# Kernel optimization log

Hardware: AMD Instinct MI355X
Metric: run time of the kernel (lower is better)

The kernel has to match this reference:

```python
import jax, jax.numpy as jnp
import numpy as np

L, B, S, C, H, V = 12, 2, 1024, 768, 12, 50257
D = C // H
FF = 4 * C
SCALE = 1.0 / float(np.sqrt(D))


def setup_inputs() -> dict:
    key = jax.random.key(0)
    ks = jax.random.split(key, 10)
    s = 0.02  # GPT-2 init std
    return {
        "idx": jax.random.randint(ks[0], (B, S), 0, V),
        "targets": jax.random.randint(ks[1], (B, S), 0, V),
        "wte": jax.random.normal(ks[2], (V, C), jnp.float32) * s,
        "wpe": jax.random.normal(ks[3], (S, C), jnp.float32) * s,
        "ln1_w": jnp.ones((L, C), jnp.float32),
        "ln1_b": jnp.zeros((L, C), jnp.float32),
        "qkv_w": jax.random.normal(ks[4], (L, C, 3 * C), jnp.float32) * s,
        "qkv_b": jnp.zeros((L, 3 * C), jnp.float32),
        "proj_w": jax.random.normal(ks[5], (L, C, C), jnp.float32) * s,
        "proj_b": jnp.zeros((L, C), jnp.float32),
        "ln2_w": jnp.ones((L, C), jnp.float32),
        "ln2_b": jnp.zeros((L, C), jnp.float32),
        "fc_w": jax.random.normal(ks[6], (L, C, FF), jnp.float32) * s,
        "fc_b": jnp.zeros((L, FF), jnp.float32),
        "fc2_w": jax.random.normal(ks[7], (L, FF, C), jnp.float32) * s,
        "fc2_b": jnp.zeros((L, C), jnp.float32),
        "lnf_w": jnp.ones((C,), jnp.float32),
        "lnf_b": jnp.zeros((C,), jnp.float32),
    }


def _ln(x, w, b):
    m = jnp.mean(x, axis=-1, keepdims=True)
    v = jnp.mean(jnp.square(x - m), axis=-1, keepdims=True)
    return (x - m) * jax.lax.rsqrt(v + 1e-5) * w + b


def _gpt(wte, wpe, ln1_w, ln1_b, qkv_w, qkv_b, proj_w, proj_b,
         ln2_w, ln2_b, fc_w, fc_b, fc2_w, fc2_b, lnf_w, lnf_b, idx, targets):
    h = wte[idx] + wpe[jnp.arange(S)]  # [B,S,C]
    causal = jnp.tril(jnp.ones((S, S), bool))

    def block(h, p):
        l1w, l1b, qw, qb, pw, pb, l2w, l2b, fw, fb, gw, gb = p
        x = _ln(h, l1w, l1b)
        q, k, v = jnp.split(x @ qw + qb, 3, axis=-1)  # each [B,S,C]
        heads = lambda t: t.reshape(B, S, H, D).transpose(0, 2, 1, 3)  # [B,H,S,D]
        q, k, v = heads(q), heads(k), heads(v)
        scores = jnp.einsum('bhsd,bhtd->bhst', q, k) * SCALE
        scores = jnp.where(causal, scores, -jnp.inf)
        att = jax.nn.softmax(scores, axis=-1)
        o = jnp.einsum('bhst,bhtd->bhsd', att, v)
        o = o.transpose(0, 2, 1, 3).reshape(B, S, C)
        h = h + o @ pw + pb
        x = _ln(h, l2w, l2b)
        h = h + jax.nn.gelu(x @ fw + fb, approximate=True) @ gw + gb
        return h, None

    h, _ = jax.lax.scan(block, h, (ln1_w, ln1_b, qkv_w, qkv_b, proj_w, proj_b,
                                   ln2_w, ln2_b, fc_w, fc_b, fc2_w, fc2_b))
    logits = _ln(h, lnf_w, lnf_b) @ wte.T  # tied lm_head, [B,S,V]
    logp = jax.nn.log_softmax(logits, axis=-1)
    loss = -jnp.mean(jnp.take_along_axis(logp, targets[..., None], axis=-1))
    return logits, loss


def reference(idx, targets, wte, wpe, ln1_w, ln1_b, qkv_w, qkv_b, proj_w, proj_b,
              ln2_w, ln2_b, fc_w, fc_b, fc2_w, fc2_b, lnf_w, lnf_b):
    return _gpt(wte, wpe, ln1_w, ln1_b, qkv_w, qkv_b, proj_w, proj_b,
                ln2_w, ln2_b, fc_w, fc_b, fc2_w, fc2_b, lnf_w, lnf_b, idx, targets)
```

## Files before the change

### kernel.cpp

```cpp
#include <hip/hip_runtime.h>
#include <hip/hip_bf16.h>
#include <cstdint>
#include <cstddef>

constexpr int LNUM = 12;
constexpr int BB   = 2;
constexpr int SS   = 1024;
constexpr int CC   = 768;
constexpr int HH   = 12;
constexpr int DD   = 64;
constexpr int FFD  = 3072;
constexpr int VV   = 50257;
constexpr int VPAD = 50304;
constexpr int MM   = BB * SS;
constexpr int NBX  = VPAD / 128;

typedef unsigned short u16;
typedef short     s16x8 __attribute__((ext_vector_type(8)));
typedef float     f32x4 __attribute__((ext_vector_type(4)));
typedef u16       u16x4 __attribute__((ext_vector_type(4)));
typedef u16       u16x8 __attribute__((ext_vector_type(8)));

__device__ __forceinline__ float bf2f(u16 v) {
    return __uint_as_float(((unsigned)v) << 16);
}
__device__ __forceinline__ u16 f2bf(float f) {
    unsigned u = __float_as_uint(f);
    return (u16)((u + 0x7fffu + ((u >> 16) & 1u)) >> 16);
}


__global__ __launch_bounds__(256) void wte_conv_kernel(const float* __restrict__ wte,
                                                       u16* __restrict__ out) {
    size_t i4 = ((size_t)blockIdx.x * 256 + threadIdx.x) * 4;
    if (i4 >= (size_t)VPAD * CC) return;
    size_t r = i4 / CC;
    u16x4 o;
    if (r < (size_t)VV) {
        const float4 v = *(const float4*)&wte[i4];
        o[0] = f2bf(v.x); o[1] = f2bf(v.y); o[2] = f2bf(v.z); o[3] = f2bf(v.w);
    } else {
        o[0] = o[1] = o[2] = o[3] = 0;
    }
    *(u16x4*)&out[i4] = o;
}

__global__ __launch_bounds__(256) void transpose_conv_kernel(const float* __restrict__ in,
                                                             u16* __restrict__ out,
                                                             int R, int Cn) {
    __shared__ float tile[32][33];
    const float* inp = in + (size_t)blockIdx.z * R * Cn;
    u16* outp = out + (size_t)blockIdx.z * R * Cn;
    int c  = blockIdx.x * 32 + threadIdx.x;
    int r0 = blockIdx.y * 32;
#pragma unroll
    for (int i = 0; i < 4; ++i) {
        int r = r0 + threadIdx.y + i * 8;
        tile[threadIdx.y + i * 8][threadIdx.x] = inp[(size_t)r * Cn + c];
    }
    __syncthreads();
    int oc = r0 + threadIdx.x;
#pragma unroll
    for (int i = 0; i < 4; ++i) {
        int orow = blockIdx.x * 32 + threadIdx.y + i * 8;
        outp[(size_t)orow * R + oc] = f2bf(tile[threadIdx.x][threadIdx.y + i * 8]);
    }
}

__global__ __launch_bounds__(256) void embed_kernel(const int* __restrict__ idx,
                                                    const float* __restrict__ wte,
                                                    const float* __restrict__ wpe,
                                                    float* __restrict__ h) {
    int row = blockIdx.x;
    int s   = row & (SS - 1);
    int tok = idx[row];
    const float* we = wte + (size_t)tok * CC;
    const float* pe = wpe + (size_t)s * CC;
    float* hr = h + (size_t)row * CC;
    for (int c = threadIdx.x; c < CC; c += 256) hr[c] = we[c] + pe[c];
}

__global__ __launch_bounds__(256) void ln_kernel(const float* __restrict__ h,
                                                 const float* __restrict__ w,
                                                 const float* __restrict__ b,
                                                 u16* __restrict__ x) {
    int row = blockIdx.x, tid = threadIdx.x;
    const float* hr = h + (size_t)row * CC;
    float v0 = hr[tid], v1 = hr[tid + 256], v2 = hr[tid + 512];
    float s  = v0 + v1 + v2;
    float s2 = v0 * v0 + v1 * v1 + v2 * v2;
#pragma unroll
    for (int off = 32; off; off >>= 1) {
        s  += __shfl_xor(s, off);
        s2 += __shfl_xor(s2, off);
    }
    __shared__ float rs[4], rs2[4], stat[2];
    int wid = tid >> 6;
    if ((tid & 63) == 0) { rs[wid] = s; rs2[wid] = s2; }
    __syncthreads();
    if (tid == 0) {
        float ts  = rs[0] + rs[1] + rs[2] + rs[3];
        float ts2 = rs2[0] + rs2[1] + rs2[2] + rs2[3];
        float mean = ts * (1.0f / CC);
        float var  = ts2 * (1.0f / CC) - mean * mean;
        stat[0] = mean;
        stat[1] = rsqrtf(var + 1e-5f);
    }
    __syncthreads();
    float mean = stat[0], rstd = stat[1];
    size_t base = (size_t)row * CC;
    x[base + tid]       = f2bf((v0 - mean) * rstd * w[tid]       + b[tid]);
    x[base + tid + 256] = f2bf((v1 - mean) * rstd * w[tid + 256] + b[tid + 256]);
    x[base + tid + 512] = f2bf((v2 - mean) * rstd * w[tid + 512] + b[tid + 512]);
}

template <int BM, int BN, int EPI>
__global__ __launch_bounds__(256)
void gemm_bt_kernel(const u16* __restrict__ A, const u16* __restrict__ Bt,
                    const float* __restrict__ bias, float* __restrict__ outf,
                    u16* __restrict__ outb, int K, long long ldo,
                    float* __restrict__ partM, float* __restrict__ partS) {
    constexpr int MR  = BM / 32, NR = BN / 32;
    constexpr int ACH = BM * 64 / (256 * 8);
    constexpr int BCH = BN * 64 / (256 * 8);
    __shared__ u16 As[BM * 64];
    __shared__ u16 Bs[BN * 64];
    const int tid  = threadIdx.x;
    const int lane = tid & 63;
    const int wid  = tid >> 6;
    const int l15  = lane & 15;
    const int lq   = lane >> 4;
    const int wm   = wid & 1;
    const int wn   = wid >> 1;
    const int rx   = l15 & 7;

    const int gx = gridDim.x, gy = gridDim.y;
    const int nwg = gx * gy;
    const int pos = blockIdx.y * gx + blockIdx.x;
    const int qc  = nwg >> 3, rc = nwg & 7;
    const int xcd = pos & 7, cidx = pos >> 3;
    const int wgid = (xcd < rc ? xcd * (qc + 1) : rc * (qc + 1) + (xcd - rc) * qc) + cidx;
    const int bx = wgid / gy, by = wgid % gy;
    const int bm0 = by * BM, bn0 = bx * BN;

    f32x4 acc[MR][NR];
#pragma unroll
    for (int m = 0; m < MR; ++m)
#pragma unroll
        for (int n = 0; n < NR; ++n) acc[m][n] = (f32x4){0.f, 0.f, 0.f, 0.f};

    u16x8 areg[ACH], breg[BCH];
    auto ldreg = [&](int kt) {
#pragma unroll
        for (int it = 0; it < ACH; ++it) {
            int g = it * 256 + tid, r = g >> 3, c = ((g & 7) ^ (r & 7)) * 8;
            areg[it] = *(const u16x8*)&A[(size_t)(bm0 + r) * (size_t)K + kt + c];
        }
#pragma unroll
        for (int it = 0; it < BCH; ++it) {
            int g = it * 256 + tid, r = g >> 3, c = ((g & 7) ^ (r & 7)) * 8;
            breg[it] = *(const u16x8*)&Bt[(size_t)(bn0 + r) * (size_t)K + kt + c];
        }
    };
    auto wlds = [&]() {
#pragma unroll
        for (int it = 0; it < ACH; ++it) *(u16x8*)&As[(it * 256 + tid) * 8] = areg[it];
#pragma unroll
        for (int it = 0; it < BCH; ++it) *(u16x8*)&Bs[(it * 256 + tid) * 8] = breg[it];
    };
    auto compute = [&]() {
#pragma unroll
        for (int ks = 0; ks < 2; ++ks) {
            s16x8 af[MR], bfr[NR];
#pragma unroll
            for (int m = 0; m < MR; ++m) {
                int row = wm * (BM / 2) + m * 16 + l15;
                af[m] = *(const s16x8*)&As[row * 64 + (((ks * 4 + lq) ^ rx) * 8)];
            }
#pragma unroll
            for (int n = 0; n < NR; ++n) {
                int row = wn * (BN / 2) + n * 16 + l15;
                bfr[n] = *(const s16x8*)&Bs[row * 64 + (((ks * 4 + lq) ^ rx) * 8)];
            }
#pragma unroll
            for (int m = 0; m < MR; ++m)
#pragma unroll
                for (int n = 0; n < NR; ++n)
                    acc[m][n] = __builtin_amdgcn_mfma_f32_16x16x32_bf16(af[m], bfr[n], acc[m][n], 0, 0, 0);
        }
    };

    const int nk = K >> 6;
    ldreg(0);
    for (int t = 0; t < nk; ++t) {
        __syncthreads();
        wlds();
        __syncthreads();
        if (t + 1 < nk) ldreg((t + 1) << 6);
        compute();
    }

#pragma unroll
    for (int m = 0; m < MR; ++m) {
#pragma unroll
        for (int n = 0; n < NR; ++n) {
#pragma unroll
            for (int r = 0; r < 4; ++r) {
                int row = bm0 + wm * (BM / 2) + m * 16 + lq * 4 + r;
                int col = bn0 + wn * (BN / 2) + n * 16 + l15;
                float v = acc[m][n][r];
                if (EPI != 3) v += bias[col];
                if (EPI == 1) {
                    float xg = v;
                    v = 0.5f * xg * (1.0f + tanhf(0.7978845608028654f * (xg + 0.044715f * xg * xg * xg)));
                }
                if (EPI == 0 || EPI == 1) {
                    outb[(size_t)row * ldo + col] = f2bf(v);
                } else if (EPI == 2) {
                    outf[(size_t)row * ldo + col] += v;
                } else {
                    if (col < VV) outf[(size_t)row * ldo + col] = v;
                }
            }
        }
    }

    if constexpr (EPI == 3) {
        __shared__ float redM[2][BM], redS[2][BM];
#pragma unroll
        for (int m = 0; m < MR; ++m) {
#pragma unroll
            for (int r = 0; r < 4; ++r) {
                float mx = -3.0e38f;
#pragma unroll
                for (int n = 0; n < NR; ++n) {
                    int colg = bn0 + wn * (BN / 2) + n * 16 + l15;
                    float v = (colg < VV) ? acc[m][n][r] : -3.0e38f;
                    mx = fmaxf(mx, v);
                }
#pragma unroll
                for (int off = 1; off < 16; off <<= 1) mx = fmaxf(mx, __shfl_xor(mx, off));
                float sm = 0.f;
#pragma unroll
                for (int n = 0; n < NR; ++n) {
                    int colg = bn0 + wn * (BN / 2) + n * 16 + l15;
                    if (colg < VV) sm += __expf(acc[m][n][r] - mx);
                }
#pragma unroll
                for (int off = 1; off < 16; off <<= 1) sm += __shfl_xor(sm, off);
                if (l15 == 0) {
                    int rl = wm * (BM / 2) + m * 16 + lq * 4 + r;
                    redM[wn][rl] = mx;
                    redS[wn][rl] = sm;
                }
            }
        }
        __syncthreads();
        if (tid < BM) {
            float m0 = redM[0][tid], m1 = redM[1][tid];
            float M = fmaxf(m0, m1);
            float S = redS[0][tid] * __expf(m0 - M) + redS[1][tid] * __expf(m1 - M);
            size_t rowg = (size_t)(bm0 + tid);
            partM[rowg * NBX + bx] = M;
            partS[rowg * NBX + bx] = S;
        }
    }
}

__global__ __launch_bounds__(256) void attn_mfma_kernel(const u16* __restrict__ qkv,
                                                        u16* __restrict__ o) {
    constexpr int KB = 64, PADC = 72;
    __shared__ u16 Ks[KB][PADC];
    __shared__ u16 Vs[DD][PADC];
    __shared__ u16 Ps[4][16][PADC];

    const int tid = threadIdx.x, lane = tid & 63, wid = tid >> 6;
    const int l15 = lane & 15, lq = lane >> 4;
    const int blk = blockIdx.x;
    const int q0  = (blk & (SS / 64 - 1)) * 64;
    const int bh  = blk / (SS / 64);
    const int b   = bh / HH, hh = bh % HH;

    const size_t base = (size_t)b * SS * (3 * CC);
    const u16* qp = qkv + base + hh * DD;
    const u16* kp = qkv + base + CC + hh * DD;
    const u16* vp = qkv + base + 2 * CC + hh * DD;

    s16x8 qf[2];
    {
        const u16* qr = qp + (size_t)(q0 + wid * 16 + l15) * (3 * CC);
        qf[0] = *(const s16x8*)&qr[lq * 8];
        qf[1] = *(const s16x8*)&qr[32 + lq * 8];
    }

    float m[4], lsum[4];
    f32x4 acc_o[4];
#pragma unroll
    for (int r = 0; r < 4; ++r) { m[r] = -3.0e38f; lsum[r] = 0.f; }
#pragma unroll
    for (int nd = 0; nd < 4; ++nd) acc_o[nd] = (f32x4){0.f, 0.f, 0.f, 0.f};

    const int tend = q0 + 64;
    for (int t0 = 0; t0 < tend; t0 += KB) {
        __syncthreads();
#pragma unroll
        for (int it = 0; it < 2; ++it) {
            int g = it * 256 + tid;
            int t = g >> 3, dc = g & 7;
            *(u16x8*)&Ks[t][dc * 8] = *(const u16x8*)&kp[(size_t)(t0 + t) * (3 * CC) + dc * 8];
        }
#pragma unroll
        for (int it = 0; it < 2; ++it) {
            int g = it * 256 + tid;
            int t = g >> 3, dc = g & 7;
            u16x8 v = *(const u16x8*)&vp[(size_t)(t0 + t) * (3 * CC) + dc * 8];
#pragma unroll
            for (int e = 0; e < 8; ++e) Vs[dc * 8 + e][t] = v[e];
        }
        __syncthreads();

        f32x4 acc_s[4];
#pragma unroll
        for (int n = 0; n < 4; ++n) acc_s[n] = (f32x4){0.f, 0.f, 0.f, 0.f};
#pragma unroll
        for (int ks = 0; ks < 2; ++ks) {
#pragma unroll
            for (int n = 0; n < 4; ++n) {
                s16x8 kb = *(const s16x8*)&Ks[n * 16 + l15][ks * 32 + lq * 8];
                acc_s[n] = __builtin_amdgcn_mfma_f32_16x16x32_bf16(qf[ks], kb, acc_s[n], 0, 0, 0);
            }
        }

#pragma unroll
        for (int n = 0; n < 4; ++n) {
            int colg = t0 + n * 16 + l15;
#pragma unroll
            for (int r = 0; r < 4; ++r) {
                int rowg = q0 + wid * 16 + lq * 4 + r;
                float sv = acc_s[n][r] * 0.125f;
                acc_s[n][r] = (colg <= rowg) ? sv : -3.0e38f;
            }
        }
        float mt[4];
#pragma unroll
        for (int r = 0; r < 4; ++r)
            mt[r] = fmaxf(fmaxf(acc_s[0][r], acc_s[1][r]), fmaxf(acc_s[2][r], acc_s[3][r]));
#pragma unroll
        for (int off = 1; off < 16; off <<= 1)
#pragma unroll
            for (int r = 0; r < 4; ++r) mt[r] = fmaxf(mt[r], __shfl_xor(mt[r], off));

        float rs[4];
#pragma unroll
        for (int r = 0; r < 4; ++r) {
            float mn  = fmaxf(m[r], mt[r]);
            float scl = __expf(m[r] - mn);
            m[r] = mn;
            float ps = 0.f;
#pragma unroll
            for (int n = 0; n < 4; ++n) {
                float p = __expf(acc_s[n][r] - mn);
                acc_s[n][r] = p;
                ps += p;
            }
            rs[r] = ps;
            lsum[r] *= scl;
#pragma unroll
            for (int nd = 0; nd < 4; ++nd) acc_o[nd][r] *= scl;
        }
#pragma unroll
        for (int off = 1; off < 16; off <<= 1)
#pragma unroll
            for (int r = 0; r < 4; ++r) rs[r] += __shfl_xor(rs[r], off);
#pragma unroll
        for (int r = 0; r < 4; ++r) lsum[r] += rs[r];

#pragma unroll
        for (int n = 0; n < 4; ++n)
#pragma unroll
            for (int r = 0; r < 4; ++r)
                Ps[wid][lq * 4 + r][n * 16 + l15] = f2bf(acc_s[n][r]);
        __syncthreads();

#pragma unroll
        for (int ks = 0; ks < 2; ++ks) {
            s16x8 pa = *(const s16x8*)&Ps[wid][l15][ks * 32 + lq * 8];
#pragma unroll
            for (int nd = 0; nd < 4; ++nd) {
                s16x8 vb = *(const s16x8*)&Vs[nd * 16 + l15][ks * 32 + lq * 8];
                acc_o[nd] = __builtin_amdgcn_mfma_f32_16x16x32_bf16(pa, vb, acc_o[nd], 0, 0, 0);
            }
        }
    }

#pragma unroll
    for (int r = 0; r < 4; ++r) {
        float inv = 1.f / lsum[r];
        int rowg = q0 + wid * 16 + lq * 4 + r;
        u16* orow = o + ((size_t)b * SS + rowg) * CC + hh * DD;
#pragma unroll
        for (int nd = 0; nd < 4; ++nd)
            orow[nd * 16 + l15] = f2bf(acc_o[nd][r] * inv);
    }
}

__global__ __launch_bounds__(256) void lse_kernel(const float* __restrict__ partM,
                                                  const float* __restrict__ partS,
                                                  const float* __restrict__ logits,
                                                  const int* __restrict__ tgt,
                                                  float* __restrict__ lossp) {
    int row = blockIdx.x, tid = threadIdx.x;
    float m = -3.0e38f, s = 0.f;
    for (int i = tid; i < NBX; i += 256) {
        float pm = partM[(size_t)row * NBX + i];
        float ps = partS[(size_t)row * NBX + i];
        float nm = fmaxf(m, pm);
        s = s * __expf(m - nm) + ps * __expf(pm - nm);
        m = nm;
    }
#pragma unroll
    for (int off = 32; off; off >>= 1) {
        float om = __shfl_xor(m, off), os = __shfl_xor(s, off);
        float nm = fmaxf(m, om);
        s = s * __expf(m - nm) + os * __expf(om - nm);
        m = nm;
    }
    __shared__ float rm[4], rsh[4];
    int wid = tid >> 6;
    if ((tid & 63) == 0) { rm[wid] = m; rsh[wid] = s; }
    __syncthreads();
    if (tid == 0) {
        float M = fmaxf(fmaxf(rm[0], rm[1]), fmaxf(rm[2], rm[3]));
        float S = rsh[0] * __expf(rm[0] - M) + rsh[1] * __expf(rm[1] - M) +
                  rsh[2] * __expf(rm[2] - M) + rsh[3] * __expf(rm[3] - M);
        float lse = M + __logf(S);
        lossp[row] = lse - logits[(size_t)row * VV + tgt[row]];
    }
}

__global__ __launch_bounds__(256) void loss_reduce_kernel(const float* __restrict__ lossp,
                                                          float* __restrict__ out) {
    int tid = threadIdx.x;
    float s = 0.f;
    for (int i = tid; i < MM; i += 256) s += lossp[i];
#pragma unroll
    for (int off = 32; off; off >>= 1) s += __shfl_xor(s, off);
    __shared__ float r[4];
    if ((tid & 63) == 0) r[tid >> 6] = s;
    __syncthreads();
    if (tid == 0) out[0] = (r[0] + r[1] + r[2] + r[3]) * (1.0f / MM);
}

extern "C" void kernel_launch(void* const* d_in, const int* in_sizes, int n_in,
                              void* d_out, int out_size, void* d_ws, size_t ws_size,
                              hipStream_t stream) {
    const int*   idx     = (const int*)  d_in[0];
    const int*   targets = (const int*)  d_in[1];
    const float* wte     = (const float*)d_in[2];
    const float* wpe     = (const float*)d_in[3];
    const float* ln1w    = (const float*)d_in[4];
    const float* ln1b    = (const float*)d_in[5];
    const float* qkvw    = (const float*)d_in[6];
    const float* qkvbi   = (const float*)d_in[7];
    const float* projw   = (const float*)d_in[8];
    const float* projbi  = (const float*)d_in[9];
    const float* ln2w    = (const float*)d_in[10];
    const float* ln2b    = (const float*)d_in[11];
    const float* fcw     = (const float*)d_in[12];
    const float* fcbi    = (const float*)d_in[13];
    const float* fc2w    = (const float*)d_in[14];
    const float* fc2bi   = (const float*)d_in[15];
    const float* lnfw    = (const float*)d_in[16];
    const float* lnfb    = (const float*)d_in[17];
    float* logits = (float*)d_out;

    char* wsb = (char*)d_ws;
    size_t off = 0;
    auto alloc = [&](size_t n) -> char* {
        char* p = wsb + off;
        off = (off + n + 255) & ~(size_t)255;
        return p;
    };
    u16*   wteT  = (u16*)  alloc((size_t)VPAD * CC * 2);
    u16*   qkvT  = (u16*)  alloc((size_t)LNUM * 3 * CC * CC * 2);
    u16*   projT = (u16*)  alloc((size_t)LNUM * CC * CC * 2);
    u16*   fcT   = (u16*)  alloc((size_t)LNUM * FFD * CC * 2);
    u16*   fc2T  = (u16*)  alloc((size_t)LNUM * CC * FFD * 2);
    float* h     = (float*)alloc((size_t)MM * CC * 4);
    u16*   xb    = (u16*)  alloc((size_t)MM * CC * 2);
    u16*   qkvb  = (u16*)  alloc((size_t)MM * 3 * CC * 2);
    u16*   ob    = (u16*)  alloc((size_t)MM * CC * 2);
    u16*   gb    = (u16*)  alloc((size_t)MM * FFD * 2);
    float* lossp = (float*)alloc((size_t)MM * 4);
    float* partM = (float*)alloc((size_t)MM * NBX * 4);
    float* partS = (float*)alloc((size_t)MM * NBX * 4);

    {
        int blocks = (int)(((size_t)VPAD * CC / 4 + 255) / 256);
        wte_conv_kernel<<<blocks, 256, 0, stream>>>(wte, wteT);
    }
    transpose_conv_kernel<<<dim3(3 * CC / 32, CC / 32, LNUM), dim3(32, 8), 0, stream>>>(qkvw, qkvT, CC, 3 * CC);
    transpose_conv_kernel<<<dim3(CC / 32, CC / 32, LNUM),     dim3(32, 8), 0, stream>>>(projw, projT, CC, CC);
    transpose_conv_kernel<<<dim3(FFD / 32, CC / 32, LNUM),    dim3(32, 8), 0, stream>>>(fcw, fcT, CC, FFD);
    transpose_conv_kernel<<<dim3(CC / 32, FFD / 32, LNUM),    dim3(32, 8), 0, stream>>>(fc2w, fc2T, FFD, CC);

    embed_kernel<<<MM, 256, 0, stream>>>(idx, wte, wpe, h);

    for (int l = 0; l < LNUM; ++l) {
        const u16* qkvT_l  = qkvT  + (size_t)l * 3 * CC * CC;
        const u16* projT_l = projT + (size_t)l * CC * CC;
        const u16* fcT_l   = fcT   + (size_t)l * FFD * CC;
        const u16* fc2T_l  = fc2T  + (size_t)l * CC * FFD;

        ln_kernel<<<MM, 256, 0, stream>>>(h, ln1w + (size_t)l * CC, ln1b + (size_t)l * CC, xb);
        gemm_bt_kernel<128, 128, 0><<<dim3(3 * CC / 128, MM / 128), 256, 0, stream>>>(
            xb, qkvT_l, qkvbi + (size_t)l * 3 * CC, nullptr, qkvb, CC, 3 * CC, nullptr, nullptr);
        attn_mfma_kernel<<<BB * HH * (SS / 64), 256, 0, stream>>>(qkvb, ob);
        gemm_bt_kernel<64, 64, 2><<<dim3(CC / 64, MM / 64), 256, 0, stream>>>(
            ob, projT_l, projbi + (size_t)l * CC, h, nullptr, CC, CC, nullptr, nullptr);
        ln_kernel<<<MM, 256, 0, stream>>>(h, ln2w + (size_t)l * CC, ln2b + (size_t)l * CC, xb);
        gemm_bt_kernel<128, 128, 1><<<dim3(FFD / 128, MM / 128), 256, 0, stream>>>(
            xb, fcT_l, fcbi + (size_t)l * FFD, nullptr, gb, CC, FFD, nullptr, nullptr);
        gemm_bt_kernel<64, 64, 2><<<dim3(CC / 64, MM / 64), 256, 0, stream>>>(
            gb, fc2T_l, fc2bi + (size_t)l * CC, h, nullptr, FFD, CC, nullptr, nullptr);
    }

    ln_kernel<<<MM, 256, 0, stream>>>(h, lnfw, lnfb, xb);
    gemm_bt_kernel<128, 128, 3><<<dim3(VPAD / 128, MM / 128), 256, 0, stream>>>(
        xb, wteT, nullptr, logits, nullptr, CC, VV, partM, partS);

    lse_kernel<<<MM, 256, 0, stream>>>(partM, partS, logits, targets, lossp);
    loss_reduce_kernel<<<1, 256, 0, stream>>>(lossp, logits + (size_t)MM * VV);
}
```

Before: 2.285 ms.

## Pair causal query tiles per block and pre-transpose V for attention

Each attention block now handles two query tiles, j and 15-j, so every block does the same amount of causal work, and both tiles share each K/V tile staged in LDS. A separate kernel transposes V into a [bh][D][S] buffer through a swizzled shared tile. This removes the scalar transpose stores that used to fill Vs on every iteration. The cost is an extra launch and buffer, only 192 blocks (half as many), and more registers per thread.

```diff
diff --git a/kernel.cpp b/kernel.cpp
--- a/kernel.cpp
+++ b/kernel.cpp
@@ -267,89 +267,102 @@
     }
 }
 
-__global__ __launch_bounds__(256) void attn_mfma_kernel(const u16* __restrict__ qkv,
-                                                        u16* __restrict__ o) {
-    constexpr int KB = 64, PADC = 72;
-    __shared__ u16 Ks[KB][PADC];
-    __shared__ u16 Vs[DD][PADC];
-    __shared__ u16 Ps[4][16][PADC];
+__global__ __launch_bounds__(256) void vtrans_kernel(const u16* __restrict__ qkv,
+                                                     u16* __restrict__ vT) {
+    __shared__ u16 T[64 * 64];
+    const int tid = threadIdx.x;
+    const int t0  = blockIdx.x * 64;
+    const int bh  = blockIdx.y;
+    const int b   = bh / HH, hh = bh % HH;
+    const u16* vp = qkv + (size_t)b * SS * (3 * CC) + 2 * CC + hh * DD;
+#pragma unroll
+    for (int it = 0; it < 2; ++it) {
+        int g = it * 256 + tid;
+        int t = g >> 3, dg = g & 7;
+        u16x8 v = *(const u16x8*)&vp[(size_t)(t0 + t) * (3 * CC) + dg * 8];
+        *(u16x8*)&T[(t * 8 + (dg ^ (t & 7))) * 8] = v;
+    }
+    __syncthreads();
+    u16* op = vT + (size_t)bh * DD * SS + t0;
+#pragma unroll
+    for (int it = 0; it < 2; ++it) {
+        int g = it * 256 + tid;
+        int d = g >> 3, tc = g & 7;
+        u16x8 o;
+#pragma unroll
+        for (int e = 0; e < 8; ++e) {
+            int t = tc * 8 + e;
+            o[e] = T[(t * 8 + ((d >> 3) ^ (t & 7))) * 8 + (d & 7)];
+        }
+        *(u16x8*)&op[(size_t)d * SS + tc * 8] = o;
+    }
+}
+
+__global__ __launch_bounds__(256) void attn_mfma2_kernel(const u16* __restrict__ qkv,
+                                                         const u16* __restrict__ vT,
+                                                         u16* __restrict__ o) {
+    constexpr int PADC = 72;
+    __shared__ u16 Ks[64][PADC];
+    __shared__ u16 Vs[64][PADC];
+    __shared__ u16 Ps[4][2][16][PADC];
 
     const int tid = threadIdx.x, lane = tid & 63, wid = tid >> 6;
     const int l15 = lane & 15, lq = lane >> 4;
-    const int blk = blockIdx.x;
-    const int q0  = (blk & (SS / 64 - 1)) * 64;
-    const int bh  = blk / (SS / 64);
+    const int pos = blockIdx.x;
+    const int bh  = (pos & 7) + 8 * ((pos >> 3) >> 3);
+    const int jlo = (pos >> 3) & 7;
+    const int jhi = 15 - jlo;
     const int b   = bh / HH, hh = bh % HH;
+    const int q0lo = jlo * 64, q0hi = jhi * 64;
 
     const size_t base = (size_t)b * SS * (3 * CC);
-    const u16* qp = qkv + base + hh * DD;
     const u16* kp = qkv + base + CC + hh * DD;
-    const u16* vp = qkv + base + 2 * CC + hh * DD;
-
-    s16x8 qf[2];
+    const u16* vp = vT + (size_t)bh * DD * SS;
+
+    s16x8 qA[2], qB[2];
     {
-        const u16* qr = qp + (size_t)(q0 + wid * 16 + l15) * (3 * CC);
-        qf[0] = *(const s16x8*)&qr[lq * 8];
-        qf[1] = *(const s16x8*)&qr[32 + lq * 8];
-    }
-
-    float m[4], lsum[4];
-    f32x4 acc_o[4];
-#pragma unroll
-    for (int r = 0; r < 4; ++r) { m[r] = -3.0e38f; lsum[r] = 0.f; }
-#pragma unroll
-    for (int nd = 0; nd < 4; ++nd) acc_o[nd] = (f32x4){0.f, 0.f, 0.f, 0.f};
-
-    const int tend = q0 + 64;
-    for (int t0 = 0; t0 < tend; t0 += KB) {
-        __syncthreads();
-#pragma unroll
-        for (int it = 0; it < 2; ++it) {
-            int g = it * 256 + tid;
-            int t = g >> 3, dc = g & 7;
-            *(u16x8*)&Ks[t][dc * 8] = *(const u16x8*)&kp[(size_t)(t0 + t) * (3 * CC) + dc * 8];
-        }
-#pragma unroll
-        for (int it = 0; it < 2; ++it) {
-            int g = it * 256 + tid;
-            int t = g >> 3, dc = g & 7;
-            u16x8 v = *(const u16x8*)&vp[(size_t)(t0 + t) * (3 * CC) + dc * 8];
-#pragma unroll
-            for (int e = 0; e < 8; ++e) Vs[dc * 8 + e][t] = v[e];
-        }
-        __syncthreads();
-
-        f32x4 acc_s[4];
-#pragma unroll
-        for (int n = 0; n < 4; ++n) acc_s[n] = (f32x4){0.f, 0.f, 0.f, 0.f};
-#pragma unroll
-        for (int ks = 0; ks < 2; ++ks) {
+        const u16* qr = qkv + base + hh * DD + (size_t)(q0hi + wid * 16 + l15) * (3 * CC);
+        qA[0] = *(const s16x8*)&qr[lq * 8];
+        qA[1] = *(const s16x8*)&qr[32 + lq * 8];
+        const u16* qr2 = qkv + base + hh * DD + (size_t)(q0lo + wid * 16 + l15) * (3 * CC);
+        qB[0] = *(const s16x8*)&qr2[lq * 8];
+        qB[1] = *(const s16x8*)&qr2[32 + lq * 8];
+    }
+
+    float mA[4], lA[4], mB[4], lB[4];
+    f32x4 oA[4], oB[4];
+#pragma unroll
+    for (int r = 0; r < 4; ++r) { mA[r] = mB[r] = -3.0e38f; lA[r] = lB[r] = 0.f; }
+#pragma unroll
+    for (int nd = 0; nd < 4; ++nd) { oA[nd] = (f32x4){0.f,0.f,0.f,0.f}; oB[nd] = (f32x4){0.f,0.f,0.f,0.f}; }
+
+    auto smax = [&](f32x4 (&sc)[4], float (&m)[4], float (&lsum)[4], f32x4 (&acc)[4],
+                    int ptile, int rowq0, bool diag, int t0) {
+        if (diag) {
 #pragma unroll
             for (int n = 0; n < 4; ++n) {
-                s16x8 kb = *(const s16x8*)&Ks[n * 16 + l15][ks * 32 + lq * 8];
-                acc_s[n] = __builtin_amdgcn_mfma_f32_16x16x32_bf16(qf[ks], kb, acc_s[n], 0, 0, 0);
-            }
-        }
-
-#pragma unroll
-        for (int n = 0; n < 4; ++n) {
-            int colg = t0 + n * 16 + l15;
-#pragma unroll
-            for (int r = 0; r < 4; ++r) {
-                int rowg = q0 + wid * 16 + lq * 4 + r;
-                float sv = acc_s[n][r] * 0.125f;
-                acc_s[n][r] = (colg <= rowg) ? sv : -3.0e38f;
-            }
+                int colg = t0 + n * 16 + l15;
+#pragma unroll
+                for (int r = 0; r < 4; ++r) {
+                    int rowg = rowq0 + wid * 16 + lq * 4 + r;
+                    float sv = sc[n][r] * 0.125f;
+                    sc[n][r] = (colg <= rowg) ? sv : -3.0e38f;
+                }
+            }
+        } else {
+#pragma unroll
+            for (int n = 0; n < 4; ++n)
+#pragma unroll
+                for (int r = 0; r < 4; ++r) sc[n][r] *= 0.125f;
         }
         float mt[4];
 #pragma unroll
         for (int r = 0; r < 4; ++r)
-            mt[r] = fmaxf(fmaxf(acc_s[0][r], acc_s[1][r]), fmaxf(acc_s[2][r], acc_s[3][r]));
+            mt[r] = fmaxf(fmaxf(sc[0][r], sc[1][r]), fmaxf(sc[2][r], sc[3][r]));
 #pragma unroll
         for (int off = 1; off < 16; off <<= 1)
 #pragma unroll
             for (int r = 0; r < 4; ++r) mt[r] = fmaxf(mt[r], __shfl_xor(mt[r], off));
-
         float rs[4];
 #pragma unroll
         for (int r = 0; r < 4; ++r) {
@@ -359,14 +372,14 @@
             float ps = 0.f;
 #pragma unroll
             for (int n = 0; n < 4; ++n) {
-                float p = __expf(acc_s[n][r] - mn);
-                acc_s[n][r] = p;
+                float p = __expf(sc[n][r] - mn);
+                sc[n][r] = p;
                 ps += p;
             }
             rs[r] = ps;
             lsum[r] *= scl;
 #pragma unroll
-            for (int nd = 0; nd < 4; ++nd) acc_o[nd][r] *= scl;
+            for (int nd = 0; nd < 4; ++nd) acc[nd][r] *= scl;
         }
 #pragma unroll
         for (int off = 1; off < 16; off <<= 1)
@@ -374,34 +387,80 @@
             for (int r = 0; r < 4; ++r) rs[r] += __shfl_xor(rs[r], off);
 #pragma unroll
         for (int r = 0; r < 4; ++r) lsum[r] += rs[r];
-
 #pragma unroll
         for (int n = 0; n < 4; ++n)
 #pragma unroll
             for (int r = 0; r < 4; ++r)
-                Ps[wid][lq * 4 + r][n * 16 + l15] = f2bf(acc_s[n][r]);
+                Ps[wid][ptile][lq * 4 + r][n * 16 + l15] = f2bf(sc[n][r]);
+    };
+
+    for (int tt = 0; tt <= jhi; ++tt) {
+        const int t0 = tt * 64;
+        const bool dolo = (tt <= jlo);
         __syncthreads();
-
+#pragma unroll
+        for (int it = 0; it < 2; ++it) {
+            int g = it * 256 + tid;
+            int r = g >> 3, c = (g & 7) * 8;
+            *(u16x8*)&Ks[r][c] = *(const u16x8*)&kp[(size_t)(t0 + r) * (3 * CC) + c];
+            *(u16x8*)&Vs[r][c] = *(const u16x8*)&vp[(size_t)r * SS + t0 + c];
+        }
+        __syncthreads();
+
+        f32x4 sA[4], sB[4];
+#pragma unroll
+        for (int n = 0; n < 4; ++n) { sA[n] = (f32x4){0.f,0.f,0.f,0.f}; sB[n] = (f32x4){0.f,0.f,0.f,0.f}; }
 #pragma unroll
         for (int ks = 0; ks < 2; ++ks) {
-            s16x8 pa = *(const s16x8*)&Ps[wid][l15][ks * 32 + lq * 8];
-#pragma unroll
-            for (int nd = 0; nd < 4; ++nd) {
-                s16x8 vb = *(const s16x8*)&Vs[nd * 16 + l15][ks * 32 + lq * 8];
-                acc_o[nd] = __builtin_amdgcn_mfma_f32_16x16x32_bf16(pa, vb, acc_o[nd], 0, 0, 0);
-            }
-        }
-    }
-
-#pragma unroll
-    for (int r = 0; r < 4; ++r) {
-        float inv = 1.f / lsum[r];
-        int rowg = q0 + wid * 16 + lq * 4 + r;
-        u16* orow = o + ((size_t)b * SS + rowg) * CC + hh * DD;
-#pragma unroll
-        for (int nd = 0; nd < 4; ++nd)
-            orow[nd * 16 + l15] = f2bf(acc_o[nd][r] * inv);
-    }
+            s16x8 kb[4];
+#pragma unroll
+            for (int n = 0; n < 4; ++n)
+                kb[n] = *(const s16x8*)&Ks[n * 16 + l15][ks * 32 + lq * 8];
+#pragma unroll
+            for (int n = 0; n < 4; ++n)
+                sA[n] = __builtin_amdgcn_mfma_f32_16x16x32_bf16(qA[ks], kb[n], sA[n], 0, 0, 0);
+            if (dolo) {
+#pragma unroll
+                for (int n = 0; n < 4; ++n)
+                    sB[n] = __builtin_amdgcn_mfma_f32_16x16x32_bf16(qB[ks], kb[n], sB[n], 0, 0, 0);
+            }
+        }
+
+        smax(sA, mA, lA, oA, 0, q0hi, tt == jhi, t0);
+        if (dolo) smax(sB, mB, lB, oB, 1, q0lo, tt == jlo, t0);
+
+#pragma unroll
+        for (int ks = 0; ks < 2; ++ks) {
+            s16x8 vb[4];
+#pragma unroll
+            for (int nd = 0; nd < 4; ++nd)
+                vb[nd] = *(const s16x8*)&Vs[nd * 16 + l15][ks * 32 + lq * 8];
+            s16x8 paA = *(const s16x8*)&Ps[wid][0][l15][ks * 32 + lq * 8];
+#pragma unroll
+            for (int nd = 0; nd < 4; ++nd)
+                oA[nd] = __builtin_amdgcn_mfma_f32_16x16x32_bf16(paA, vb[nd], oA[nd], 0, 0, 0);
+            if (dolo) {
+                s16x8 paB = *(const s16x8*)&Ps[wid][1][l15][ks * 32 + lq * 8];
+#pragma unroll
+                for (int nd = 0; nd < 4; ++nd)
+                    oB[nd] = __builtin_amdgcn_mfma_f32_16x16x32_bf16(paB, vb[nd], oB[nd], 0, 0, 0);
+            }
+        }
+    }
+
+    auto writeO = [&](float (&lsum)[4], f32x4 (&acc)[4], int rowq0) {
+#pragma unroll
+        for (int r = 0; r < 4; ++r) {
+            float inv = 1.f / lsum[r];
+            int rowg = rowq0 + wid * 16 + lq * 4 + r;
+            u16* orow = o + ((size_t)b * SS + rowg) * CC + hh * DD;
+#pragma unroll
+            for (int nd = 0; nd < 4; ++nd)
+                orow[nd * 16 + l15] = f2bf(acc[nd][r] * inv);
+        }
+    };
+    writeO(lA, oA, q0hi);
+    writeO(lB, oB, q0lo);
 }
 
 __global__ __launch_bounds__(256) void lse_kernel(const float* __restrict__ partM,
@@ -491,6 +550,7 @@
     u16*   qkvb  = (u16*)  alloc((size_t)MM * 3 * CC * 2);
     u16*   ob    = (u16*)  alloc((size_t)MM * CC * 2);
     u16*   gb    = (u16*)  alloc((size_t)MM * FFD * 2);
+    u16*   vTb   = (u16*)  alloc((size_t)BB * HH * DD * SS * 2);
     float* lossp = (float*)alloc((size_t)MM * 4);
     float* partM = (float*)alloc((size_t)MM * NBX * 4);
     float* partS = (float*)alloc((size_t)MM * NBX * 4);
@@ -515,7 +575,8 @@
         ln_kernel<<<MM, 256, 0, stream>>>(h, ln1w + (size_t)l * CC, ln1b + (size_t)l * CC, xb);
         gemm_bt_kernel<128, 128, 0><<<dim3(3 * CC / 128, MM / 128), 256, 0, stream>>>(
             xb, qkvT_l, qkvbi + (size_t)l * 3 * CC, nullptr, qkvb, CC, 3 * CC, nullptr, nullptr);
-        attn_mfma_kernel<<<BB * HH * (SS / 64), 256, 0, stream>>>(qkvb, ob);
+        vtrans_kernel<<<dim3(SS / 64, BB * HH), 256, 0, stream>>>(qkvb, vTb);
+        attn_mfma2_kernel<<<BB * HH * 8, 256, 0, stream>>>(qkvb, vTb, ob);
         gemm_bt_kernel<64, 64, 2><<<dim3(CC / 64, MM / 64), 256, 0, stream>>>(
             ob, projT_l, projbi + (size_t)l * CC, h, nullptr, CC, CC, nullptr, nullptr);
         ln_kernel<<<MM, 256, 0, stream>>>(h, ln2w + (size_t)l * CC, ln2b + (size_t)l * CC, xb);
```

Measured after the change: 2.085 ms. 8.7% less time.

## Pre-transpose V in a separate kernel and schedule causal attention heaviest-first

Applied to the files above, without the earlier changes.

Adds a small kernel that writes V per head in transposed [D,S] layout through an XOR-swizzled shared tile. Attention can then load V tiles with vectorized row copies instead of scattering scalar transposed stores into shared memory for every key tile of every query block. The attention kernel also launches the longest causal query blocks first, applies the causal mask only on the diagonal tile, and drops the block barrier after the per-wave P store. In exchange it adds one extra launch and a V round trip through global memory per layer. Removing that barrier relies on each wave only reading the P rows it wrote itself.

```diff
diff --git a/kernel.cpp b/kernel.cpp
--- a/kernel.cpp
+++ b/kernel.cpp
@@ -12,8 +12,8 @@
 constexpr int FFD  = 3072;
 constexpr int VV   = 50257;
 constexpr int VPAD = 50304;
+constexpr int NBX  = VPAD / 128;
 constexpr int MM   = BB * SS;
-constexpr int NBX  = VPAD / 128;
 
 typedef unsigned short u16;
 typedef short     s16x8 __attribute__((ext_vector_type(8)));
@@ -267,28 +267,60 @@
     }
 }
 
-__global__ __launch_bounds__(256) void attn_mfma_kernel(const u16* __restrict__ qkv,
-                                                        u16* __restrict__ o) {
-    constexpr int KB = 64, PADC = 72;
-    __shared__ u16 Ks[KB][PADC];
-    __shared__ u16 Vs[DD][PADC];
+__global__ __launch_bounds__(256) void vtrans_kernel(const u16* __restrict__ qkv,
+                                                     u16* __restrict__ vT) {
+    __shared__ u16 T[64 * 64];
+    const int tid = threadIdx.x;
+    const int t0  = blockIdx.x * 64;
+    const int bh  = blockIdx.y;
+    const int b   = bh / HH, hh = bh % HH;
+    const u16* vp = qkv + (size_t)b * SS * (3 * CC) + 2 * CC + hh * DD;
+#pragma unroll
+    for (int it = 0; it < 2; ++it) {
+        int g = it * 256 + tid;
+        int t = g >> 3, dg = g & 7;
+        u16x8 v = *(const u16x8*)&vp[(size_t)(t0 + t) * (3 * CC) + dg * 8];
+        *(u16x8*)&T[(t * 8 + (dg ^ (t & 7))) * 8] = v;
+    }
+    __syncthreads();
+    u16* op = vT + (size_t)bh * DD * SS + t0;
+#pragma unroll
+    for (int it = 0; it < 2; ++it) {
+        int g = it * 256 + tid;
+        int d = g >> 3, tc = g & 7;
+        u16x8 o;
+#pragma unroll
+        for (int e = 0; e < 8; ++e) {
+            int t = tc * 8 + e;
+            o[e] = T[(t * 8 + ((d >> 3) ^ (t & 7))) * 8 + (d & 7)];
+        }
+        *(u16x8*)&op[(size_t)d * SS + tc * 8] = o;
+    }
+}
+
+__global__ __launch_bounds__(256) void attn_mfma3_kernel(const u16* __restrict__ qkv,
+                                                         const u16* __restrict__ vT,
+                                                         u16* __restrict__ o) {
+    constexpr int PADC = 72;
+    __shared__ u16 Ks[64][PADC];
+    __shared__ u16 Vs[64][PADC];
     __shared__ u16 Ps[4][16][PADC];
 
     const int tid = threadIdx.x, lane = tid & 63, wid = tid >> 6;
     const int l15 = lane & 15, lq = lane >> 4;
-    const int blk = blockIdx.x;
-    const int q0  = (blk & (SS / 64 - 1)) * 64;
-    const int bh  = blk / (SS / 64);
+    const int pos = blockIdx.x;
+    const int j   = 15 - pos / 24;
+    const int bh  = pos % 24;
     const int b   = bh / HH, hh = bh % HH;
+    const int q0  = j * 64;
 
     const size_t base = (size_t)b * SS * (3 * CC);
-    const u16* qp = qkv + base + hh * DD;
     const u16* kp = qkv + base + CC + hh * DD;
-    const u16* vp = qkv + base + 2 * CC + hh * DD;
+    const u16* vp = vT + (size_t)bh * DD * SS;
 
     s16x8 qf[2];
     {
-        const u16* qr = qp + (size_t)(q0 + wid * 16 + l15) * (3 * CC);
+        const u16* qr = qkv + base + hh * DD + (size_t)(q0 + wid * 16 + l15) * (3 * CC);
         qf[0] = *(const s16x8*)&qr[lq * 8];
         qf[1] = *(const s16x8*)&qr[32 + lq * 8];
     }
@@ -300,56 +332,56 @@
 #pragma unroll
     for (int nd = 0; nd < 4; ++nd) acc_o[nd] = (f32x4){0.f, 0.f, 0.f, 0.f};
 
-    const int tend = q0 + 64;
-    for (int t0 = 0; t0 < tend; t0 += KB) {
+    for (int tt = 0; tt <= j; ++tt) {
+        const int t0 = tt * 64;
         __syncthreads();
 #pragma unroll
         for (int it = 0; it < 2; ++it) {
             int g = it * 256 + tid;
-            int t = g >> 3, dc = g & 7;
-            *(u16x8*)&Ks[t][dc * 8] = *(const u16x8*)&kp[(size_t)(t0 + t) * (3 * CC) + dc * 8];
-        }
-#pragma unroll
-        for (int it = 0; it < 2; ++it) {
-            int g = it * 256 + tid;
-            int t = g >> 3, dc = g & 7;
-            u16x8 v = *(const u16x8*)&vp[(size_t)(t0 + t) * (3 * CC) + dc * 8];
-#pragma unroll
-            for (int e = 0; e < 8; ++e) Vs[dc * 8 + e][t] = v[e];
+            int r = g >> 3, c = (g & 7) * 8;
+            *(u16x8*)&Ks[r][c] = *(const u16x8*)&kp[(size_t)(t0 + r) * (3 * CC) + c];
+            *(u16x8*)&Vs[r][c] = *(const u16x8*)&vp[(size_t)r * SS + t0 + c];
         }
         __syncthreads();
 
-        f32x4 acc_s[4];
-#pragma unroll
-        for (int n = 0; n < 4; ++n) acc_s[n] = (f32x4){0.f, 0.f, 0.f, 0.f};
+        f32x4 sc[4];
+#pragma unroll
+        for (int n = 0; n < 4; ++n) sc[n] = (f32x4){0.f, 0.f, 0.f, 0.f};
 #pragma unroll
         for (int ks = 0; ks < 2; ++ks) {
 #pragma unroll
             for (int n = 0; n < 4; ++n) {
                 s16x8 kb = *(const s16x8*)&Ks[n * 16 + l15][ks * 32 + lq * 8];
-                acc_s[n] = __builtin_amdgcn_mfma_f32_16x16x32_bf16(qf[ks], kb, acc_s[n], 0, 0, 0);
-            }
-        }
-
-#pragma unroll
-        for (int n = 0; n < 4; ++n) {
-            int colg = t0 + n * 16 + l15;
-#pragma unroll
-            for (int r = 0; r < 4; ++r) {
-                int rowg = q0 + wid * 16 + lq * 4 + r;
-                float sv = acc_s[n][r] * 0.125f;
-                acc_s[n][r] = (colg <= rowg) ? sv : -3.0e38f;
-            }
-        }
+                sc[n] = __builtin_amdgcn_mfma_f32_16x16x32_bf16(qf[ks], kb, sc[n], 0, 0, 0);
+            }
+        }
+
+        if (tt == j) {
+#pragma unroll
+            for (int n = 0; n < 4; ++n) {
+                int colg = t0 + n * 16 + l15;
+#pragma unroll
+                for (int r = 0; r < 4; ++r) {
+                    int rowg = q0 + wid * 16 + lq * 4 + r;
+                    float sv = sc[n][r] * 0.125f;
+                    sc[n][r] = (colg <= rowg) ? sv : -3.0e38f;
+                }
+            }
+        } else {
+#pragma unroll
+            for (int n = 0; n < 4; ++n)
+#pragma unroll
+                for (int r = 0; r < 4; ++r) sc[n][r] *= 0.125f;
+        }
+
         float mt[4];
 #pragma unroll
         for (int r = 0; r < 4; ++r)
-            mt[r] = fmaxf(fmaxf(acc_s[0][r], acc_s[1][r]), fmaxf(acc_s[2][r], acc_s[3][r]));
+            mt[r] = fmaxf(fmaxf(sc[0][r], sc[1][r]), fmaxf(sc[2][r], sc[3][r]));
 #pragma unroll
         for (int off = 1; off < 16; off <<= 1)
 #pragma unroll
             for (int r = 0; r < 4; ++r) mt[r] = fmaxf(mt[r], __shfl_xor(mt[r], off));
-
         float rs[4];
 #pragma unroll
         for (int r = 0; r < 4; ++r) {
@@ -359,8 +391,8 @@
             float ps = 0.f;
 #pragma unroll
             for (int n = 0; n < 4; ++n) {
-                float p = __expf(acc_s[n][r] - mn);
-                acc_s[n][r] = p;
+                float p = __expf(sc[n][r] - mn);
+                sc[n][r] = p;
                 ps += p;
             }
             rs[r] = ps;
@@ -379,8 +411,7 @@
         for (int n = 0; n < 4; ++n)
 #pragma unroll
             for (int r = 0; r < 4; ++r)
-                Ps[wid][lq * 4 + r][n * 16 + l15] = f2bf(acc_s[n][r]);
-        __syncthreads();
+                Ps[wid][lq * 4 + r][n * 16 + l15] = f2bf(sc[n][r]);
 
 #pragma unroll
         for (int ks = 0; ks < 2; ++ks) {
@@ -491,6 +522,7 @@
     u16*   qkvb  = (u16*)  alloc((size_t)MM * 3 * CC * 2);
     u16*   ob    = (u16*)  alloc((size_t)MM * CC * 2);
     u16*   gb    = (u16*)  alloc((size_t)MM * FFD * 2);
+    u16*   vTb   = (u16*)  alloc((size_t)BB * HH * DD * SS * 2);
     float* lossp = (float*)alloc((size_t)MM * 4);
     float* partM = (float*)alloc((size_t)MM * NBX * 4);
     float* partS = (float*)alloc((size_t)MM * NBX * 4);
@@ -515,7 +547,8 @@
         ln_kernel<<<MM, 256, 0, stream>>>(h, ln1w + (size_t)l * CC, ln1b + (size_t)l * CC, xb);
         gemm_bt_kernel<128, 128, 0><<<dim3(3 * CC / 128, MM / 128), 256, 0, stream>>>(
             xb, qkvT_l, qkvbi + (size_t)l * 3 * CC, nullptr, qkvb, CC, 3 * CC, nullptr, nullptr);
-        attn_mfma_kernel<<<BB * HH * (SS / 64), 256, 0, stream>>>(qkvb, ob);
+        vtrans_kernel<<<dim3(SS / 64, BB * HH), 256, 0, stream>>>(qkvb, vTb);
+        attn_mfma3_kernel<<<BB * HH * 16, 256, 0, stream>>>(qkvb, vTb, ob);
         gemm_bt_kernel<64, 64, 2><<<dim3(CC / 64, MM / 64), 256, 0, stream>>>(
             ob, projT_l, projbi + (size_t)l * CC, h, nullptr, CC, CC, nullptr, nullptr);
         ln_kernel<<<MM, 256, 0, stream>>>(h, ln2w + (size_t)l * CC, ln2b + (size_t)l * CC, xb);
```

Result: faster. 2.052 ms (-10.2%).
